# Performance work log

Hardware: AMD Instinct MI355X
Metric: run time of the kernel (lower is better)

## Reference

```python
import jax, jax.numpy as jnp
import numpy as np

NEG_SLOPE = 0.2
MASK_FILL = -9e10


def setup_inputs() -> dict:
    key = jax.random.key(0)
    ks = jax.random.split(key, 8)
    B, N, D = 8, 2048, 64
    return {
        "opes_mask_adj": jax.random.randint(ks[0], (B, N, N), 0, 2, dtype=jnp.int32),
        "opes_mask_job": jax.random.randint(ks[1], (B, N, N), 0, 2, dtype=jnp.int32),
        "batch_idxes": jnp.arange(B, dtype=jnp.int64),
        "feats": jax.random.normal(ks[2], (B, N, D), dtype=jnp.float32),
        "W_ope": jax.random.normal(ks[3], (D, D), dtype=jnp.float32) * (1.0 / np.sqrt(D)),
        "attn_src": jax.random.normal(ks[4], (D,), dtype=jnp.float32) * (1.0 / np.sqrt(D)),
        "attn_dst": jax.random.normal(ks[5], (D,), dtype=jnp.float32) * (1.0 / np.sqrt(D)),
        "lambda_params": jax.random.normal(ks[6], (D, 2), dtype=jnp.float32),
    }


def reference(opes_mask_adj, opes_mask_job, batch_idxes, feats, W_ope, attn_src, attn_dst, lambda_params):
    # h_ope: [B, N, D]  (Linear with weight [out,in]: x @ W^T)
    h_ope = jnp.einsum("bnd,od->bno", feats, W_ope)
    a_src = h_ope @ attn_src  # [B, N]
    a_dst = h_ope @ attn_dst  # [B, N]
    e = a_src[:, :, None] + a_dst[:, None, :]  # [B, N, N]
    e = jnp.where(e >= 0, e, NEG_SLOPE * e)  # leaky relu

    mask_adj = opes_mask_adj[batch_idxes] == 1
    alpha_adj = jax.nn.softmax(jnp.where(mask_adj, e, MASK_FILL), axis=-1)
    h_adj = jnp.einsum("bnm,bmd->bnd", alpha_adj, h_ope)

    mask_job = opes_mask_job[batch_idxes] == 1
    alpha_job = jax.nn.softmax(jnp.where(mask_job, e, MASK_FILL), axis=-1)
    h_job = jnp.einsum("bnm,bmd->bnd", alpha_job, h_ope)

    # in_dim == out_dim -> identity residual (res_fc is None)
    lambdas = jax.nn.softmax(lambda_params, axis=1)  # [D, 2]
    lambda_adj, lambda_job = lambdas[:, 0], lambdas[:, 1]
    return lambda_adj * h_adj + lambda_job * h_job + feats
```

## Files before the change

### kernel.cpp

```cpp
#include <hip/hip_runtime.h>
#include <hip/hip_bf16.h>

#define B_ 8
#define N_ 2048
#define D_ 64

typedef __attribute__((ext_vector_type(8))) short bf16x8;
typedef __attribute__((ext_vector_type(4))) float f32x4;

__device__ inline unsigned short f32_bf16_rne(float f) {
    unsigned u = __float_as_uint(f);
    u += 0x7fffu + ((u >> 16) & 1u);
    return (unsigned short)(u >> 16);
}

__global__ __launch_bounds__(256) void prep_kernel(
    const float* __restrict__ feats, const float* __restrict__ W,
    const float* __restrict__ attn_src, const float* __restrict__ attn_dst,
    unsigned short* __restrict__ hT, float* __restrict__ a_src,
    float* __restrict__ a_dst) {
    __shared__ float w_lds[64 * 65];
    __shared__ float f_lds[32 * 64];
    __shared__ unsigned short hT_lds[64 * 40];

    const int t = threadIdx.x;
    const int b = blockIdx.x >> 6;
    const int rowbase = (blockIdx.x & 63) * 32;

#pragma unroll
    for (int k = 0; k < 4; k++) {
        int lin = (k * 256 + t) * 4;
        float4 v = *(const float4*)(W + lin);
        int o = lin >> 6, d = lin & 63;
        float* p = &w_lds[o * 65 + d];
        p[0] = v.x; p[1] = v.y; p[2] = v.z; p[3] = v.w;
    }
#pragma unroll
    for (int k = 0; k < 2; k++) {
        int lin = (k * 256 + t) * 4;
        float4 v = *(const float4*)(feats + (size_t)(b * N_ + rowbase) * D_ + lin);
        float* p = &f_lds[lin];
        p[0] = v.x; p[1] = v.y; p[2] = v.z; p[3] = v.w;
    }
    __syncthreads();

    const int w = t >> 6;
    const int o = t & 63;
    float acc[8] = {0.f, 0.f, 0.f, 0.f, 0.f, 0.f, 0.f, 0.f};
#pragma unroll 8
    for (int d = 0; d < 64; d++) {
        float wv = w_lds[o * 65 + d];
#pragma unroll
        for (int rr = 0; rr < 8; rr++)
            acc[rr] = fmaf(f_lds[(w * 8 + rr) * 64 + d], wv, acc[rr]);
    }
    float as_ = attn_src[o], ad_ = attn_dst[o];
#pragma unroll
    for (int rr = 0; rr < 8; rr++) {
        int row = rowbase + w * 8 + rr;
        float s1 = acc[rr] * as_;
        float s2 = acc[rr] * ad_;
#pragma unroll
        for (int off = 32; off; off >>= 1) {
            s1 += __shfl_xor(s1, off);
            s2 += __shfl_xor(s2, off);
        }
        if (o == 0) {
            a_src[b * N_ + row] = s1;
            a_dst[b * N_ + row] = s2;
        }
        hT_lds[o * 40 + w * 8 + rr] = f32_bf16_rne(acc[rr]);
    }
    __syncthreads();
    const int d = t >> 2, seg = t & 3;
    uint4 vv = *(const uint4*)(&hT_lds[d * 40 + seg * 8]);
    *(uint4*)(hT + ((size_t)(b * 64 + d) * N_ + rowbase + seg * 8)) = vv;
}

__global__ __launch_bounds__(256) void attn_kernel(
    const int* __restrict__ mask_adj, const int* __restrict__ mask_job,
    const int* __restrict__ batch_idxes,
    const unsigned short* __restrict__ hT, const float* __restrict__ a_src,
    const float* __restrict__ a_dst, const float* __restrict__ feats,
    const float* __restrict__ lambda_params, float* __restrict__ out) {
    __shared__ unsigned short hstage[64 * 128];

    const int t = threadIdx.x;
    const int b = blockIdx.x >> 5;
    const int ibase = (blockIdx.x & 31) * 64;
    const int wid = t >> 6, lane = t & 63;
    const int m = lane & 15, q = lane >> 4;
    const int irow0 = ibase + wid * 16;
    const int i_a = irow0 + m;

    int bi = batch_idxes[b];
    bi = (bi < 0) ? 0 : ((bi >= B_) ? (B_ - 1) : bi);
    const int* mA = mask_adj + (size_t)bi * N_ * N_ + (size_t)i_a * N_;
    const int* mJ = mask_job + (size_t)bi * N_ * N_ + (size_t)i_a * N_;
    const float asrc = a_src[b * N_ + i_a];
    const float* adst = a_dst + b * N_;

    f32x4 accA[4], accJ[4];
#pragma unroll
    for (int dd = 0; dd < 4; dd++) {
        accA[dd] = (f32x4){0.f, 0.f, 0.f, 0.f};
        accJ[dd] = (f32x4){0.f, 0.f, 0.f, 0.f};
    }
    float zA = 0.f, zJ = 0.f;

    const int sd = t >> 2, sseg = t & 3;
    const unsigned short* hrow = hT + (size_t)(b * 64 + sd) * N_;

    for (int jt = 0; jt < N_ / 128; jt++) {
        const int j0 = jt * 128;
#pragma unroll
        for (int c = 0; c < 4; c++) {
            int jc = sseg * 4 + c;
            uint4 v = *(const uint4*)(hrow + j0 + jc * 8);
            *(uint4*)(hstage + (sd * 16 + (jc ^ (sd & 15))) * 8) = v;
        }
        __syncthreads();

#pragma unroll
        for (int kk = 0; kk < 4; kk++) {
            const int jl = j0 + kk * 32 + q * 8;
            int4 a0 = *(const int4*)(mA + jl);
            int4 a1 = *(const int4*)(mA + jl + 4);
            int4 b0 = *(const int4*)(mJ + jl);
            int4 b1 = *(const int4*)(mJ + jl + 4);
            float4 d0 = *(const float4*)(adst + jl);
            float4 d1 = *(const float4*)(adst + jl + 4);
            int ma[8] = {a0.x, a0.y, a0.z, a0.w, a1.x, a1.y, a1.z, a1.w};
            int mj[8] = {b0.x, b0.y, b0.z, b0.w, b1.x, b1.y, b1.z, b1.w};
            float dv[8] = {d0.x, d0.y, d0.z, d0.w, d1.x, d1.y, d1.z, d1.w};
            bf16x8 fa, fj;
#pragma unroll
            for (int tt = 0; tt < 8; tt++) {
                float e = asrc + dv[tt];
                float le = fmaxf(e, 0.f) + 0.2f * fminf(e, 0.f);
                float p = __expf(le);
                float pa = (ma[tt] == 1) ? p : 0.f;
                float pj = (mj[tt] == 1) ? p : 0.f;
                zA += pa;
                zJ += pj;
                fa[tt] = (short)f32_bf16_rne(pa);
                fj[tt] = (short)f32_bf16_rne(pj);
            }
#pragma unroll
            for (int dd = 0; dd < 4; dd++) {
                int dn = dd * 16 + m;
                int jcl = kk * 4 + q;
                bf16x8 fb = *(const bf16x8*)(hstage +
                                (dn * 16 + (jcl ^ (dn & 15))) * 8);
                accA[dd] = __builtin_amdgcn_mfma_f32_16x16x32_bf16(fa, fb, accA[dd], 0, 0, 0);
                accJ[dd] = __builtin_amdgcn_mfma_f32_16x16x32_bf16(fj, fb, accJ[dd], 0, 0, 0);
            }
        }
        __syncthreads();
    }

    zA += __shfl_xor(zA, 16); zA += __shfl_xor(zA, 32);
    zJ += __shfl_xor(zJ, 16); zJ += __shfl_xor(zJ, 32);
    float* zbuf = (float*)hstage;
    if (q == 0) {
        zbuf[wid * 32 + m] = zA;
        zbuf[wid * 32 + 16 + m] = zJ;
    }
    __syncthreads();

    float invA[4], invJ[4];
#pragma unroll
    for (int r = 0; r < 4; r++) {
        invA[r] = 1.f / zbuf[wid * 32 + q * 4 + r];
        invJ[r] = 1.f / zbuf[wid * 32 + 16 + q * 4 + r];
    }
#pragma unroll
    for (int dd = 0; dd < 4; dd++) {
        int d = dd * 16 + m;
        float l0 = lambda_params[d * 2];
        float l1 = lambda_params[d * 2 + 1];
        float e0 = __expf(l0), e1 = __expf(l1);
        float inv = 1.f / (e0 + e1);
        float la = e0 * inv, lj = e1 * inv;
#pragma unroll
        for (int r = 0; r < 4; r++) {
            int i = irow0 + q * 4 + r;
            size_t off = (size_t)(b * N_ + i) * D_ + d;
            out[off] = la * accA[dd][r] * invA[r] + lj * accJ[dd][r] * invJ[r] + feats[off];
        }
    }
}

extern "C" void kernel_launch(void* const* d_in, const int* in_sizes, int n_in,
                              void* d_out, int out_size, void* d_ws, size_t ws_size,
                              hipStream_t stream) {
    const int* mask_adj = (const int*)d_in[0];
    const int* mask_job = (const int*)d_in[1];
    const int* batch_idxes = (const int*)d_in[2];
    const float* feats = (const float*)d_in[3];
    const float* W = (const float*)d_in[4];
    const float* attn_src = (const float*)d_in[5];
    const float* attn_dst = (const float*)d_in[6];
    const float* lambda_params = (const float*)d_in[7];
    float* out = (float*)d_out;

    unsigned short* hT = (unsigned short*)d_ws;
    float* a_src = (float*)((char*)d_ws + (size_t)B_ * 64 * N_ * 2);
    float* a_dst = a_src + B_ * N_;

    prep_kernel<<<B_ * (N_ / 32), 256, 0, stream>>>(feats, W, attn_src, attn_dst,
                                                    hT, a_src, a_dst);
    attn_kernel<<<B_ * (N_ / 64), 256, 0, stream>>>(mask_adj, mask_job, batch_idxes,
                                                    hT, a_src, a_dst, feats,
                                                    lambda_params, out);
}
```

Before: 306.2 us.

## Split attention key dimension across two wave groups per block with LDS reduction

```diff
diff --git a/kernel.cpp b/kernel.cpp
--- a/kernel.cpp
+++ b/kernel.cpp
@@ -77,28 +77,42 @@
     *(uint4*)(hT + ((size_t)(b * 64 + d) * N_ + rowbase + seg * 8)) = vv;
 }
 
-__global__ __launch_bounds__(256) void attn_kernel(
+__global__ __launch_bounds__(512, 4) void attn_kernel(
     const int* __restrict__ mask_adj, const int* __restrict__ mask_job,
     const int* __restrict__ batch_idxes,
     const unsigned short* __restrict__ hT, const float* __restrict__ a_src,
     const float* __restrict__ a_dst, const float* __restrict__ feats,
     const float* __restrict__ lambda_params, float* __restrict__ out) {
-    __shared__ unsigned short hstage[64 * 128];
+    __shared__ unsigned short hstage[2 * 64 * 128];
+    __shared__ float zb[256];
 
     const int t = threadIdx.x;
-    const int b = blockIdx.x >> 5;
-    const int ibase = (blockIdx.x & 31) * 64;
+    const int b = blockIdx.x >> 6;
+    const int ibase = (blockIdx.x & 63) * 64;
+    (void)b; (void)ibase;
+
+    const int blk = blockIdx.x;
+    const int bb = blk >> 6;
+    (void)bb;
+    const int batch = blk / 32;
+    (void)batch;
+
+    const int b2 = blockIdx.x >> 5;
+    const int ib2 = (blockIdx.x & 31) * 64;
+
     const int wid = t >> 6, lane = t & 63;
+    const int rowg = wid & 3;
+    const int jh = wid >> 2;
     const int m = lane & 15, q = lane >> 4;
-    const int irow0 = ibase + wid * 16;
+    const int irow0 = ib2 + rowg * 16;
     const int i_a = irow0 + m;
 
-    int bi = batch_idxes[b];
+    int bi = batch_idxes[b2];
     bi = (bi < 0) ? 0 : ((bi >= B_) ? (B_ - 1) : bi);
     const int* mA = mask_adj + (size_t)bi * N_ * N_ + (size_t)i_a * N_;
     const int* mJ = mask_job + (size_t)bi * N_ * N_ + (size_t)i_a * N_;
-    const float asrc = a_src[b * N_ + i_a];
-    const float* adst = a_dst + b * N_;
+    const float asrc = a_src[b2 * N_ + i_a];
+    const float* adst = a_dst + b2 * N_;
 
     f32x4 accA[4], accJ[4];
 #pragma unroll
@@ -108,16 +122,18 @@
     }
     float zA = 0.f, zJ = 0.f;
 
-    const int sd = t >> 2, sseg = t & 3;
-    const unsigned short* hrow = hT + (size_t)(b * 64 + sd) * N_;
-
-    for (int jt = 0; jt < N_ / 128; jt++) {
-        const int j0 = jt * 128;
+    const int tt_ = t & 255;
+    const int sd = tt_ >> 2, sseg = tt_ & 3;
+    const unsigned short* hrow = hT + (size_t)(b2 * 64 + sd) * N_;
+    unsigned short* hst = hstage + jh * (64 * 128);
+
+    for (int jt = 0; jt < 8; jt++) {
+        const int j0 = jh * 1024 + jt * 128;
 #pragma unroll
         for (int c = 0; c < 4; c++) {
             int jc = sseg * 4 + c;
             uint4 v = *(const uint4*)(hrow + j0 + jc * 8);
-            *(uint4*)(hstage + (sd * 16 + (jc ^ (sd & 15))) * 8) = v;
+            *(uint4*)(hst + (sd * 16 + (jc ^ (sd & 15))) * 8) = v;
         }
         __syncthreads();
 
@@ -135,23 +151,22 @@
             float dv[8] = {d0.x, d0.y, d0.z, d0.w, d1.x, d1.y, d1.z, d1.w};
             bf16x8 fa, fj;
 #pragma unroll
-            for (int tt = 0; tt < 8; tt++) {
-                float e = asrc + dv[tt];
+            for (int u = 0; u < 8; u++) {
+                float e = asrc + dv[u];
                 float le = fmaxf(e, 0.f) + 0.2f * fminf(e, 0.f);
                 float p = __expf(le);
-                float pa = (ma[tt] == 1) ? p : 0.f;
-                float pj = (mj[tt] == 1) ? p : 0.f;
+                float pa = (ma[u] == 1) ? p : 0.f;
+                float pj = (mj[u] == 1) ? p : 0.f;
                 zA += pa;
                 zJ += pj;
-                fa[tt] = (short)f32_bf16_rne(pa);
-                fj[tt] = (short)f32_bf16_rne(pj);
+                fa[u] = (short)f32_bf16_rne(pa);
+                fj[u] = (short)f32_bf16_rne(pj);
             }
 #pragma unroll
             for (int dd = 0; dd < 4; dd++) {
                 int dn = dd * 16 + m;
                 int jcl = kk * 4 + q;
-                bf16x8 fb = *(const bf16x8*)(hstage +
-                                (dn * 16 + (jcl ^ (dn & 15))) * 8);
+                bf16x8 fb = *(const bf16x8*)(hst + (dn * 16 + (jcl ^ (dn & 15))) * 8);
                 accA[dd] = __builtin_amdgcn_mfma_f32_16x16x32_bf16(fa, fb, accA[dd], 0, 0, 0);
                 accJ[dd] = __builtin_amdgcn_mfma_f32_16x16x32_bf16(fj, fb, accJ[dd], 0, 0, 0);
             }
@@ -161,32 +176,51 @@
 
     zA += __shfl_xor(zA, 16); zA += __shfl_xor(zA, 32);
     zJ += __shfl_xor(zJ, 16); zJ += __shfl_xor(zJ, 32);
-    float* zbuf = (float*)hstage;
-    if (q == 0) {
-        zbuf[wid * 32 + m] = zA;
-        zbuf[wid * 32 + 16 + m] = zJ;
-    }
-    __syncthreads();
-
-    float invA[4], invJ[4];
-#pragma unroll
-    for (int r = 0; r < 4; r++) {
-        invA[r] = 1.f / zbuf[wid * 32 + q * 4 + r];
-        invJ[r] = 1.f / zbuf[wid * 32 + 16 + q * 4 + r];
-    }
-#pragma unroll
-    for (int dd = 0; dd < 4; dd++) {
-        int d = dd * 16 + m;
-        float l0 = lambda_params[d * 2];
-        float l1 = lambda_params[d * 2 + 1];
-        float e0 = __expf(l0), e1 = __expf(l1);
-        float inv = 1.f / (e0 + e1);
-        float la = e0 * inv, lj = e1 * inv;
+
+    __syncthreads();
+    float* cbuf = (float*)hstage;
+    if (jh == 1) {
+#pragma unroll
+        for (int dd = 0; dd < 4; dd++)
+#pragma unroll
+            for (int r = 0; r < 4; r++) {
+                cbuf[(rowg * 32 + dd * 4 + r) * 64 + lane] = accA[dd][r];
+                cbuf[(rowg * 32 + 16 + dd * 4 + r) * 64 + lane] = accJ[dd][r];
+            }
+        if (q == 0) {
+            zb[128 + rowg * 16 + m] = zA;
+            zb[192 + rowg * 16 + m] = zJ;
+        }
+    } else if (q == 0) {
+        zb[rowg * 16 + m] = zA;
+        zb[64 + rowg * 16 + m] = zJ;
+    }
+    __syncthreads();
+
+    if (jh == 0) {
+        float invA[4], invJ[4];
 #pragma unroll
         for (int r = 0; r < 4; r++) {
-            int i = irow0 + q * 4 + r;
-            size_t off = (size_t)(b * N_ + i) * D_ + d;
-            out[off] = la * accA[dd][r] * invA[r] + lj * accJ[dd][r] * invJ[r] + feats[off];
+            int rw = rowg * 16 + q * 4 + r;
+            invA[r] = 1.f / (zb[rw] + zb[128 + rw]);
+            invJ[r] = 1.f / (zb[64 + rw] + zb[192 + rw]);
+        }
+#pragma unroll
+        for (int dd = 0; dd < 4; dd++) {
+            int d = dd * 16 + m;
+            float l0 = lambda_params[d * 2];
+            float l1 = lambda_params[d * 2 + 1];
+            float e0 = __expf(l0), e1 = __expf(l1);
+            float inv = 1.f / (e0 + e1);
+            float la = e0 * inv, lj = e1 * inv;
+#pragma unroll
+            for (int r = 0; r < 4; r++) {
+                int i = irow0 + q * 4 + r;
+                float vA = accA[dd][r] + cbuf[(rowg * 32 + dd * 4 + r) * 64 + lane];
+                float vJ = accJ[dd][r] + cbuf[(rowg * 32 + 16 + dd * 4 + r) * 64 + lane];
+                size_t off = (size_t)(b2 * N_ + i) * D_ + d;
+                out[off] = la * vA * invA[r] + lj * vJ * invJ[r] + feats[off];
+            }
         }
     }
 }
@@ -210,7 +244,7 @@
 
     prep_kernel<<<B_ * (N_ / 32), 256, 0, stream>>>(feats, W, attn_src, attn_dst,
                                                     hT, a_src, a_dst);
-    attn_kernel<<<B_ * (N_ / 64), 256, 0, stream>>>(mask_adj, mask_job, batch_idxes,
+    attn_kernel<<<B_ * (N_ / 64), 512, 0, stream>>>(mask_adj, mask_job, batch_idxes,
                                                     hT, a_src, a_dst, feats,
                                                     lambda_params, out);
 }
```

Result: slower. 322.1 us (+5.2%).

## Split attention key dimension across blocks and reduce partial sums in combine kernel

Applied to the files above, without the earlier changes.

```diff
diff --git a/kernel.cpp b/kernel.cpp
--- a/kernel.cpp
+++ b/kernel.cpp
@@ -81,24 +81,29 @@
     const int* __restrict__ mask_adj, const int* __restrict__ mask_job,
     const int* __restrict__ batch_idxes,
     const unsigned short* __restrict__ hT, const float* __restrict__ a_src,
-    const float* __restrict__ a_dst, const float* __restrict__ feats,
-    const float* __restrict__ lambda_params, float* __restrict__ out) {
+    const float* __restrict__ a_dst, float* __restrict__ pacc,
+    float* __restrict__ zpart) {
     __shared__ unsigned short hstage[64 * 128];
 
     const int t = threadIdx.x;
-    const int b = blockIdx.x >> 5;
-    const int ibase = (blockIdx.x & 31) * 64;
+    const int tile = blockIdx.x;
+    const int b2 = tile >> 5;
+    const int ib2 = (tile & 31) * 64;
+    const int S = gridDim.y;
+    const int jcount = (N_ / 128) / S;
+    const int j0base = blockIdx.y * jcount * 128;
+
     const int wid = t >> 6, lane = t & 63;
     const int m = lane & 15, q = lane >> 4;
-    const int irow0 = ibase + wid * 16;
+    const int irow0 = ib2 + wid * 16;
     const int i_a = irow0 + m;
 
-    int bi = batch_idxes[b];
+    int bi = batch_idxes[b2];
     bi = (bi < 0) ? 0 : ((bi >= B_) ? (B_ - 1) : bi);
     const int* mA = mask_adj + (size_t)bi * N_ * N_ + (size_t)i_a * N_;
     const int* mJ = mask_job + (size_t)bi * N_ * N_ + (size_t)i_a * N_;
-    const float asrc = a_src[b * N_ + i_a];
-    const float* adst = a_dst + b * N_;
+    const float asrc = a_src[b2 * N_ + i_a];
+    const float* adst = a_dst + b2 * N_;
 
     f32x4 accA[4], accJ[4];
 #pragma unroll
@@ -109,10 +114,10 @@
     float zA = 0.f, zJ = 0.f;
 
     const int sd = t >> 2, sseg = t & 3;
-    const unsigned short* hrow = hT + (size_t)(b * 64 + sd) * N_;
-
-    for (int jt = 0; jt < N_ / 128; jt++) {
-        const int j0 = jt * 128;
+    const unsigned short* hrow = hT + (size_t)(b2 * 64 + sd) * N_;
+
+    for (int jt = 0; jt < jcount; jt++) {
+        const int j0 = j0base + jt * 128;
 #pragma unroll
         for (int c = 0; c < 4; c++) {
             int jc = sseg * 4 + c;
@@ -135,23 +140,22 @@
             float dv[8] = {d0.x, d0.y, d0.z, d0.w, d1.x, d1.y, d1.z, d1.w};
             bf16x8 fa, fj;
 #pragma unroll
-            for (int tt = 0; tt < 8; tt++) {
-                float e = asrc + dv[tt];
+            for (int u = 0; u < 8; u++) {
+                float e = asrc + dv[u];
                 float le = fmaxf(e, 0.f) + 0.2f * fminf(e, 0.f);
                 float p = __expf(le);
-                float pa = (ma[tt] == 1) ? p : 0.f;
-                float pj = (mj[tt] == 1) ? p : 0.f;
+                float pa = (ma[u] == 1) ? p : 0.f;
+                float pj = (mj[u] == 1) ? p : 0.f;
                 zA += pa;
                 zJ += pj;
-                fa[tt] = (short)f32_bf16_rne(pa);
-                fj[tt] = (short)f32_bf16_rne(pj);
+                fa[u] = (short)f32_bf16_rne(pa);
+                fj[u] = (short)f32_bf16_rne(pj);
             }
 #pragma unroll
             for (int dd = 0; dd < 4; dd++) {
                 int dn = dd * 16 + m;
                 int jcl = kk * 4 + q;
-                bf16x8 fb = *(const bf16x8*)(hstage +
-                                (dn * 16 + (jcl ^ (dn & 15))) * 8);
+                bf16x8 fb = *(const bf16x8*)(hstage + (dn * 16 + (jcl ^ (dn & 15))) * 8);
                 accA[dd] = __builtin_amdgcn_mfma_f32_16x16x32_bf16(fa, fb, accA[dd], 0, 0, 0);
                 accJ[dd] = __builtin_amdgcn_mfma_f32_16x16x32_bf16(fj, fb, accJ[dd], 0, 0, 0);
             }
@@ -161,33 +165,78 @@
 
     zA += __shfl_xor(zA, 16); zA += __shfl_xor(zA, 32);
     zJ += __shfl_xor(zJ, 16); zJ += __shfl_xor(zJ, 32);
-    float* zbuf = (float*)hstage;
+
+    const size_t blk = (size_t)tile * S + blockIdx.y;
+    float* pb = pacc + blk * 8192;
+    float* zr = zpart + blk * 128;
     if (q == 0) {
-        zbuf[wid * 32 + m] = zA;
-        zbuf[wid * 32 + 16 + m] = zJ;
-    }
-    __syncthreads();
-
-    float invA[4], invJ[4];
-#pragma unroll
-    for (int r = 0; r < 4; r++) {
-        invA[r] = 1.f / zbuf[wid * 32 + q * 4 + r];
-        invJ[r] = 1.f / zbuf[wid * 32 + 16 + q * 4 + r];
+        zr[wid * 16 + m] = zA;
+        zr[64 + wid * 16 + m] = zJ;
     }
 #pragma unroll
     for (int dd = 0; dd < 4; dd++) {
         int d = dd * 16 + m;
-        float l0 = lambda_params[d * 2];
-        float l1 = lambda_params[d * 2 + 1];
-        float e0 = __expf(l0), e1 = __expf(l1);
-        float inv = 1.f / (e0 + e1);
-        float la = e0 * inv, lj = e1 * inv;
 #pragma unroll
         for (int r = 0; r < 4; r++) {
-            int i = irow0 + q * 4 + r;
-            size_t off = (size_t)(b * N_ + i) * D_ + d;
-            out[off] = la * accA[dd][r] * invA[r] + lj * accJ[dd][r] * invJ[r] + feats[off];
-        }
+            int i = wid * 16 + q * 4 + r;
+            pb[i * 64 + d] = accA[dd][r];
+            pb[4096 + i * 64 + d] = accJ[dd][r];
+        }
+    }
+}
+
+__global__ __launch_bounds__(256) void combine_kernel(
+    const float* __restrict__ pacc, const float* __restrict__ zpart,
+    const float* __restrict__ feats, const float* __restrict__ lambda_params,
+    float* __restrict__ out, int S) {
+    const int tile = blockIdx.x;
+    const int b = tile >> 5;
+    const int rbase = (tile & 31) * 64;
+    const int t = threadIdx.x;
+    const int i = t >> 2;
+    const int ds = (t & 3) * 16;
+
+    const float* base = pacc + (size_t)tile * S * 8192;
+    const float* zb = zpart + (size_t)tile * S * 128;
+
+    float zA = 0.f, zJ = 0.f;
+    float sA[16], sJ[16];
+#pragma unroll
+    for (int k = 0; k < 16; k++) { sA[k] = 0.f; sJ[k] = 0.f; }
+
+    for (int s = 0; s < S; s++) {
+        zA += zb[s * 128 + i];
+        zJ += zb[s * 128 + 64 + i];
+        const float* pA = base + (size_t)s * 8192 + i * 64 + ds;
+        const float* pJ = pA + 4096;
+#pragma unroll
+        for (int k4 = 0; k4 < 4; k4++) {
+            float4 vA = *(const float4*)(pA + k4 * 4);
+            float4 vJ = *(const float4*)(pJ + k4 * 4);
+            sA[k4 * 4 + 0] += vA.x; sA[k4 * 4 + 1] += vA.y;
+            sA[k4 * 4 + 2] += vA.z; sA[k4 * 4 + 3] += vA.w;
+            sJ[k4 * 4 + 0] += vJ.x; sJ[k4 * 4 + 1] += vJ.y;
+            sJ[k4 * 4 + 2] += vJ.z; sJ[k4 * 4 + 3] += vJ.w;
+        }
+    }
+    const float invA = 1.f / zA, invJ = 1.f / zJ;
+    const size_t off = ((size_t)(b * N_ + rbase + i)) * D_ + ds;
+#pragma unroll
+    for (int k4 = 0; k4 < 4; k4++) {
+        float4 f = *(const float4*)(feats + off + k4 * 4);
+        float4 o;
+        float* fo = (float*)&f;
+        float* oo = (float*)&o;
+#pragma unroll
+        for (int c = 0; c < 4; c++) {
+            int d = ds + k4 * 4 + c;
+            float e0 = __expf(lambda_params[d * 2]);
+            float e1 = __expf(lambda_params[d * 2 + 1]);
+            float inv = 1.f / (e0 + e1);
+            oo[c] = e0 * inv * sA[k4 * 4 + c] * invA +
+                    e1 * inv * sJ[k4 * 4 + c] * invJ + fo[c];
+        }
+        *(float4*)(out + off + k4 * 4) = o;
     }
 }
 
@@ -205,12 +254,28 @@
     float* out = (float*)d_out;
 
     unsigned short* hT = (unsigned short*)d_ws;
-    float* a_src = (float*)((char*)d_ws + (size_t)B_ * 64 * N_ * 2);
+    char* p = (char*)d_ws + (size_t)B_ * 64 * N_ * 2;
+    float* a_src = (float*)p;
     float* a_dst = a_src + B_ * N_;
+    char* pz = p + 2 * (size_t)B_ * N_ * 4;
+
+    auto need = [&](int S) {
+        return (size_t)(pz - (char*)d_ws) +
+               (size_t)256 * S * 128 * 4 +
+               (size_t)256 * S * 8192 * 4;
+    };
+    int S = 4;
+    if (ws_size < need(4)) S = 2;
+    if (ws_size < need(2)) S = 1;
+
+    float* zpart = (float*)pz;
+    float* pacc = zpart + (size_t)256 * S * 128;
 
     prep_kernel<<<B_ * (N_ / 32), 256, 0, stream>>>(feats, W, attn_src, attn_dst,
                                                     hT, a_src, a_dst);
-    attn_kernel<<<B_ * (N_ / 64), 256, 0, stream>>>(mask_adj, mask_job, batch_idxes,
-                                                    hT, a_src, a_dst, feats,
-                                                    lambda_params, out);
-}
+    dim3 grid(256, S, 1);
+    attn_kernel<<<grid, 256, 0, stream>>>(mask_adj, mask_job, batch_idxes,
+                                          hT, a_src, a_dst, pacc, zpart);
+    combine_kernel<<<256, 256, 0, stream>>>(pacc, zpart, feats, lambda_params,
+                                            out, S);
+}
```

Result: slower. 345.3 us (+12.8%).
